# Performance work log

Hardware: AMD Instinct MI355X
Metric: run time of the kernel (lower is better)

## Reference

```python
import jax, jax.numpy as jnp
import numpy as np

B, L, HEADS, D_HEAD = 2, 2048, 16, 64
D_MODEL = HEADS * D_HEAD            # 1024
D_BI = D_MODEL * 4 // 2             # 2048 (bilinear GLU width)
D_PROJ = D_MODEL * 3 + 2 * D_BI
DEPTH = 0                           # block depth < 2 -> token shift active
NEG_INF = -1e10


def _ln(x, g, b, eps=1e-5):
    m = jnp.mean(x, axis=-1, keepdims=True)
    v = jnp.var(x, axis=-1, keepdims=True)
    return (x - m) * jax.lax.rsqrt(v + eps) * g + b


def _shift(x, n):
    # F.pad(x, (0,0,n,-n)): shift along seq dim by n, zero-fill at front
    return jnp.pad(x, ((0, 0), (n, 0), (0, 0)))[:, : x.shape[1], :]


def setup_inputs() -> dict:
    key = jax.random.key(0)
    ks = jax.random.split(key, 3)
    x = jax.random.normal(ks[0], (B, L, D_MODEL), jnp.float32)
    w_in = jax.random.normal(ks[1], (D_MODEL, D_PROJ), jnp.float32) * (D_MODEL ** -0.5)
    # note: torch init zeros out_proj; we use small random weights so backward is non-trivial
    w_out = jax.random.normal(ks[2], (D_MODEL + D_BI, D_MODEL), jnp.float32) * 0.02
    slopes = jnp.concatenate([2.0 ** jnp.linspace(0.0, -6.0, HEADS // 2),
                              jnp.zeros(HEADS - HEADS // 2)]).astype(jnp.float32)
    return {
        "x": x,
        "in_ln_g": jnp.ones(D_MODEL, jnp.float32), "in_ln_b": jnp.zeros(D_MODEL, jnp.float32),
        "mid_ln_g": jnp.ones(D_PROJ, jnp.float32), "mid_ln_b": jnp.zeros(D_PROJ, jnp.float32),
        "out_ln_g": jnp.ones(D_MODEL, jnp.float32), "out_ln_b": jnp.zeros(D_MODEL, jnp.float32),
        "w_in": w_in, "w_out": w_out, "slopes": slopes,
    }


def reference(x, in_ln_g, in_ln_b, mid_ln_g, mid_ln_b, out_ln_g, out_ln_b, w_in, w_out, slopes):
    b, l, d = x.shape
    x = _ln(x, in_ln_g, in_ln_b)
    if DEPTH < 2:
        x = jnp.concatenate([
            _shift(x[..., : d // 4], 1),
            x[..., d // 4: d - d // 8],
            _shift(x[..., d - d // 8:], 2),
        ], axis=-1)
    h = _ln(x @ w_in, mid_ln_g, mid_ln_b)
    q, k, v, p1, p2 = jnp.split(h, [D_MODEL, 2 * D_MODEL, 3 * D_MODEL, 3 * D_MODEL + D_BI], axis=-1)
    to_heads = lambda t: t.reshape(b, l, HEADS, D_HEAD).transpose(0, 2, 1, 3)  # b h l d
    q, k, v = to_heads(q), to_heads(k), to_heads(v)
    logits = jnp.einsum('bhid,bhjd->bhij', q, k) * (D_HEAD ** -0.5)
    pos = jnp.arange(l)
    alibi = pos[None, None, None, :].astype(logits.dtype) * slopes[None, :, None, None]
    causal = jnp.where(pos[:, None] >= pos[None, :], 0.0, NEG_INF).astype(logits.dtype)
    a = jax.nn.softmax(logits + alibi + causal, axis=-1)
    o = jnp.einsum('bhij,bhjd->bhid', a, v).transpose(0, 2, 1, 3).reshape(b, l, d)
    return _ln(jnp.concatenate([o, p1 * p2], axis=-1) @ w_out, out_ln_g, out_ln_b)
```

## Files before the change

### kernel.cpp

```cpp
#include <hip/hip_runtime.h>

#define B_ 2
#define L_ 2048
#define HEADS_ 16
#define DH_ 64
#define DM_ 1024
#define DBI_ 2048
#define DPROJ_ 7168
#define NTOK (B_*L_)
#define DCAT (DM_ + DBI_)

typedef __bf16 bf16;
typedef __attribute__((ext_vector_type(8))) __bf16 bf16x8;
typedef __attribute__((ext_vector_type(4))) float floatx4;

typedef __attribute__((address_space(1))) const void gptr_t;
typedef __attribute__((address_space(3))) void lptr_t;

__device__ __forceinline__ void g2l16(const void* g, void* l) {
    __builtin_amdgcn_global_load_lds((gptr_t*)g, (lptr_t*)l, 16, 0, 0);
}

__global__ __launch_bounds__(256) void transpose_both(const float* __restrict__ w_in,
                                                      const float* __restrict__ w_out,
                                                      bf16* __restrict__ w_inT,
                                                      bf16* __restrict__ w_outT) {
    __shared__ float tile[32][33];
    int l = blockIdx.x;
    const float* in; bf16* outp; int R, C, bx, by;
    if (l < 7168) { in = w_in;  outp = w_inT;  R = DM_;  C = DPROJ_; bx = l % 224; by = l / 224; }
    else { l -= 7168; in = w_out; outp = w_outT; R = DCAT; C = DM_;   bx = l % 32;  by = l / 32; }
    int c0 = bx * 32, r0 = by * 32;
    int x = threadIdx.x & 31, y = threadIdx.x >> 5;
    for (int i = 0; i < 32; i += 8)
        tile[y + i][x] = in[(size_t)(r0 + y + i) * C + (c0 + x)];
    __syncthreads();
    for (int i = 0; i < 32; i += 8)
        outp[(size_t)(c0 + y + i) * R + (r0 + x)] = (bf16)tile[x][y + i];
}

__global__ __launch_bounds__(256) void ln_shift(const float* __restrict__ x,
                                                const float* __restrict__ g,
                                                const float* __restrict__ bb,
                                                bf16* __restrict__ xs) {
    int tok = blockIdx.x;
    int b = tok / L_, l = tok % L_;
    const float* row = x + (size_t)tok * DM_;
    float vals[4];
    float s = 0.f, s2 = 0.f;
    for (int i = 0; i < 4; i++) {
        float v = row[threadIdx.x + i * 256];
        vals[i] = v; s += v; s2 += v * v;
    }
    __shared__ float red[2][4];
    for (int o = 32; o; o >>= 1) { s += __shfl_xor(s, o); s2 += __shfl_xor(s2, o); }
    int w = threadIdx.x >> 6;
    if ((threadIdx.x & 63) == 0) { red[0][w] = s; red[1][w] = s2; }
    __syncthreads();
    s  = red[0][0] + red[0][1] + red[0][2] + red[0][3];
    s2 = red[1][0] + red[1][1] + red[1][2] + red[1][3];
    float mean = s * (1.f / DM_);
    float var  = s2 * (1.f / DM_) - mean * mean;
    float rstd = rsqrtf(var + 1e-5f);
    for (int i = 0; i < 4; i++) {
        int c = threadIdx.x + i * 256;
        float y = (vals[i] - mean) * rstd * g[c] + bb[c];
        int shift = (c < 256) ? 1 : ((c >= 896) ? 2 : 0);
        int dl = l + shift;
        if (dl < L_) xs[((size_t)b * L_ + dl) * DM_ + c] = (bf16)y;
        if (l == 0 && shift) {
            xs[((size_t)b * L_ + 0) * DM_ + c] = (bf16)0.f;
            if (shift == 2) xs[((size_t)b * L_ + 1) * DM_ + c] = (bf16)0.f;
        }
    }
}

__global__ __launch_bounds__(512, 2) void gemm1_fr(const bf16* __restrict__ A,
                                                   const bf16* __restrict__ Bt,
                                                   bf16* __restrict__ C) {
    const int K = DM_, N = DPROJ_;
    int lin = blockIdx.x;
    int xcd = lin & 7, idx = lin >> 3;
    int mt = (xcd >> 2) * 8 + idx / 7;
    int nt = (xcd & 3) * 7 + idx % 7;
    int m0 = mt * 256, n0 = nt * 256;

    __shared__ bf16 As[2][256 * 64];
    __shared__ bf16 Bs[2][256 * 64];

    int t = threadIdx.x;
    int lane = t & 63;
    int c = lane & 15, quad = lane >> 4;
    int wave = t >> 6;
    int wm = (wave >> 2) * 128;
    int wn = (wave & 3) * 64;

    auto stageA = [&](int k0, int bsel, int h) {
        #pragma unroll
        for (int s = 0; s < 2; s++) {
            int g = h * 1024 + s * 512 + t;
            int row = g >> 3;
            int kc = (g & 7) ^ (row & 7);
            g2l16(A + (size_t)(m0 + row) * K + (k0 + kc * 8), &As[bsel][g * 8]);
        }
    };
    auto stageB = [&](int k0, int bsel, int h) {
        #pragma unroll
        for (int s = 0; s < 2; s++) {
            int g = h * 1024 + s * 512 + t;
            int row = g >> 3;
            int kc = (g & 7) ^ (row & 7);
            g2l16(Bt + (size_t)(n0 + row) * K + (k0 + kc * 8), &Bs[bsel][g * 8]);
        }
    };

    floatx4 acc[8][4] = {};

    stageA(0, 0, 0); stageA(0, 0, 1);
    stageB(0, 0, 0); stageB(0, 0, 1);
    stageB(64, 1, 0); stageB(64, 1, 1);
    asm volatile("s_waitcnt vmcnt(4)" ::: "memory");
    __builtin_amdgcn_s_barrier();
    __builtin_amdgcn_sched_barrier(0);

    const int nT = K / 64;
    for (int tt = 0; tt < nT; ++tt) {
        int cur = tt & 1, nxt = cur ^ 1;
        int k1 = (tt + 1) << 6, k2 = (tt + 2) << 6;
        bool dA = (tt + 1 < nT), dB = (tt + 2 < nT);
        bf16x8 bfr[4][2];
        #pragma unroll
        for (int p = 0; p < 4; p++) {
            if      (p == 0) { if (dA) stageA(k1, nxt, 0); }
            else if (p == 1) { if (dA) stageA(k1, nxt, 1); }
            else if (p == 2) { if (dB) stageB(k2, cur, 0); }
            else             { if (dB) stageB(k2, cur, 1); }
            if (p == 0) {
                #pragma unroll
                for (int j = 0; j < 4; j++)
                    #pragma unroll
                    for (int s = 0; s < 2; s++)
                        bfr[j][s] = *(const bf16x8*)&Bs[cur][(wn + j * 16 + c) * 64
                                                            + (((s * 4 + quad) ^ (c & 7)) * 8)];
            }
            bf16x8 af[2][2];
            #pragma unroll
            for (int ii = 0; ii < 2; ii++)
                #pragma unroll
                for (int s = 0; s < 2; s++)
                    af[ii][s] = *(const bf16x8*)&As[cur][(wm + (p * 2 + ii) * 16 + c) * 64
                                                         + (((s * 4 + quad) ^ (c & 7)) * 8)];
            __builtin_amdgcn_s_setprio(1);
            #pragma unroll
            for (int ii = 0; ii < 2; ii++)
                #pragma unroll
                for (int j = 0; j < 4; j++)
                    #pragma unroll
                    for (int s = 0; s < 2; s++)
                        acc[p * 2 + ii][j] = __builtin_amdgcn_mfma_f32_16x16x32_bf16(
                            af[ii][s], bfr[j][s], acc[p * 2 + ii][j], 0, 0, 0);
            __builtin_amdgcn_s_setprio(0);
        }
        asm volatile("s_waitcnt lgkmcnt(0)" ::: "memory");
        if (dB)      { asm volatile("s_waitcnt vmcnt(4)" ::: "memory"); }
        else if (dA) { asm volatile("s_waitcnt vmcnt(0)" ::: "memory"); }
        if (tt + 1 < nT) __builtin_amdgcn_s_barrier();
        __builtin_amdgcn_sched_barrier(0);
    }

    #pragma unroll
    for (int i = 0; i < 8; i++)
        #pragma unroll
        for (int j = 0; j < 4; j++)
            #pragma unroll
            for (int r = 0; r < 4; r++) {
                int row = m0 + wm + i * 16 + quad * 4 + r;
                int col = n0 + wn + j * 16 + c;
                C[(size_t)row * N + col] = (bf16)acc[i][j][r];
            }
}

__global__ __launch_bounds__(256) void gemm2_sk(const bf16* __restrict__ A,
                                                const bf16* __restrict__ Bt,
                                                float* __restrict__ P) {
    const int ldA = DCAT, N = DM_;
    int m0 = blockIdx.x * 128, n0 = blockIdx.y * 128, kz = blockIdx.z;
    const bf16* Ak = A + kz * 1024;
    const bf16* Btk = Bt + kz * 1024;
    float* C = P + (size_t)kz * NTOK * DM_;
    __shared__ bf16 As[2][128 * 32];
    __shared__ bf16 Bs[2][128 * 32];
    int t = threadIdx.x, lane = t & 63, wave = t >> 6;
    int c = lane & 15, quad = lane >> 4;
    int wm = (wave >> 1) * 64, wn = (wave & 1) * 64;
    auto stage = [&](int k0, int bsel) {
        #pragma unroll
        for (int s = 0; s < 2; s++) {
            int f = s * 256 + t;
            int row = f >> 2, kp = (f & 3) * 8;
            g2l16(Ak + (size_t)(m0 + row) * ldA + k0 + kp, &As[bsel][f * 8]);
            g2l16(Btk + (size_t)(n0 + row) * ldA + k0 + kp, &Bs[bsel][f * 8]);
        }
    };
    floatx4 acc[4][4] = {};
    stage(0, 0);
    int buf = 0;
    for (int k0 = 0; k0 < 1024; k0 += 32) {
        __syncthreads();
        if (k0 + 32 < 1024) stage(k0 + 32, buf ^ 1);
        bf16x8 af[4], bfr[4];
        #pragma unroll
        for (int i = 0; i < 4; i++)
            af[i] = *(const bf16x8*)&As[buf][(wm + i * 16 + c) * 32 + quad * 8];
        #pragma unroll
        for (int j = 0; j < 4; j++)
            bfr[j] = *(const bf16x8*)&Bs[buf][(wn + j * 16 + c) * 32 + quad * 8];
        #pragma unroll
        for (int i = 0; i < 4; i++)
            #pragma unroll
            for (int j = 0; j < 4; j++)
                acc[i][j] = __builtin_amdgcn_mfma_f32_16x16x32_bf16(af[i], bfr[j], acc[i][j], 0, 0, 0);
        buf ^= 1;
    }
    #pragma unroll
    for (int i = 0; i < 4; i++)
        #pragma unroll
        for (int j = 0; j < 4; j++)
            #pragma unroll
            for (int r = 0; r < 4; r++) {
                int row = m0 + wm + i * 16 + quad * 4 + r;
                int col = n0 + wn + j * 16 + c;
                C[(size_t)row * N + col] = acc[i][j][r];
            }
}

__global__ __launch_bounds__(256) void mid_ln_fused(const bf16* __restrict__ h,
                                                    const float* __restrict__ g,
                                                    const float* __restrict__ bb,
                                                    bf16* __restrict__ Qp,
                                                    bf16* __restrict__ Kp,
                                                    bf16* __restrict__ Vn,
                                                    bf16* __restrict__ A2) {
    int tok = blockIdx.x;
    int b = tok >> 11, l = tok & 2047;
    size_t base = (size_t)tok * DPROJ_;
    int t = threadIdx.x;
    float v[28];
    float s = 0.f, s2 = 0.f;
    for (int i = 0; i < 28; i++) {
        v[i] = (float)h[base + t + i * 256];
        s += v[i]; s2 += v[i] * v[i];
    }
    __shared__ float red[2][4];
    for (int o = 32; o; o >>= 1) { s += __shfl_xor(s, o); s2 += __shfl_xor(s2, o); }
    int w = t >> 6;
    if ((t & 63) == 0) { red[0][w] = s; red[1][w] = s2; }
    __syncthreads();
    s  = red[0][0] + red[0][1] + red[0][2] + red[0][3];
    s2 = red[1][0] + red[1][1] + red[1][2] + red[1][3];
    float mean = s * (1.f / DPROJ_);
    float var  = s2 * (1.f / DPROJ_) - mean * mean;
    float rstd = rsqrtf(var + 1e-5f);
    #pragma unroll
    for (int i = 0; i < 28; i++) {
        int c = t + i * 256;
        v[i] = (v[i] - mean) * rstd * g[c] + bb[c];
    }
    #pragma unroll
    for (int i = 0; i < 12; i++) {
        int c = t + i * 256;
        int sec = c >> 10;
        int cc = c & 1023;
        int hh = cc >> 6, d = cc & 63;
        size_t idx = (((size_t)b * HEADS_ + hh) * L_ + l) * DH_ + d;
        bf16* dst = (sec == 0) ? Qp : (sec == 1) ? Kp : Vn;
        dst[idx] = (bf16)v[i];
    }
    #pragma unroll
    for (int i = 12; i < 20; i++) {
        int c = t + i * 256;
        A2[(size_t)tok * DCAT + DM_ + (c - 3 * DM_)] = (bf16)(v[i] * v[i + 8]);
    }
}

__global__ __launch_bounds__(256) void vt_pack(const bf16* __restrict__ Vn,
                                               bf16* __restrict__ Vt) {
    __shared__ bf16 tile[32][33];
    int bh = blockIdx.z;
    const bf16* in = Vn + (size_t)bh * L_ * DH_;
    bf16* out = Vt + (size_t)bh * DH_ * L_;
    int l0 = blockIdx.x * 32, d0 = blockIdx.y * 32;
    int x = threadIdx.x & 31, y = threadIdx.x >> 5;
    for (int i = 0; i < 32; i += 8)
        tile[y + i][x] = in[(size_t)(l0 + y + i) * DH_ + d0 + x];
    __syncthreads();
    for (int i = 0; i < 32; i += 8)
        out[(size_t)(d0 + y + i) * L_ + l0 + x] = tile[x][y + i];
}

__global__ __launch_bounds__(256, 4) void attn4(const bf16* __restrict__ Qp,
                                                const bf16* __restrict__ Kp,
                                                const bf16* __restrict__ Vt,
                                                const float* __restrict__ slopes,
                                                bf16* __restrict__ A2) {
    int hd = blockIdx.y, b = blockIdx.z;
    int lin = blockIdx.x + 32 * blockIdx.y + 512 * blockIdx.z;
    int xr = blockIdx.x;
    int qt = ((lin >> 8) & 1) ? (31 - xr) : xr;
    int q0 = qt * 64;
    int t = threadIdx.x, lane = t & 63, wave = t >> 6;
    int quad = lane >> 4, c = lane & 15;
    __shared__ bf16 Ks[2 * 64 * 32];
    __shared__ bf16 Vs[2 * 64 * 32];
    __shared__ bf16 Ps[4][16 * 72];
    int bh = b * HEADS_ + hd;
    const bf16* Qb = Qp + (size_t)bh * L_ * DH_;
    const bf16* Kb = Kp + (size_t)bh * L_ * DH_;
    const bf16* Vb = Vt + (size_t)bh * DH_ * L_;
    const float LOG2E = 1.44269504f;
    float slopeL2 = slopes[hd] * LOG2E;
    const float qscale = 0.125f * LOG2E;

    bf16x8 qf[2];
    int qrow = q0 + wave * 16 + c;
    qf[0] = *(const bf16x8*)(Qb + (size_t)qrow * DH_ + quad * 8);
    qf[1] = *(const bf16x8*)(Qb + (size_t)qrow * DH_ + 32 + quad * 8);
    floatx4 accO[4] = {};
    float lsum[4];
    float mrow[4];
    int i_row0 = q0 + wave * 16 + quad * 4;
    #pragma unroll
    for (int r = 0; r < 4; r++) {
        lsum[r] = 0.f;
        mrow[r] = slopeL2 * (float)(i_row0 + r) + 20.0f;
    }

    int row = t >> 2, kp = (t & 3) * 8;
    bf16* pw = &Ps[wave][0];
    bf16* pwr = pw + (quad * 4) * 72 + c;
    for (int j0 = 0; j0 <= q0; j0 += 64) {
        #pragma unroll
        for (int s = 0; s < 2; s++) {
            g2l16(Kb + (size_t)(j0 + row) * DH_ + s * 32 + kp, &Ks[(s * 256 + t) * 8]);
            g2l16(Vb + (size_t)row * L_ + j0 + s * 32 + kp, &Vs[(s * 256 + t) * 8]);
        }
        __syncthreads();

        bool diag = (j0 == q0);
        #pragma unroll
        for (int nt = 0; nt < 4; nt++) {
            floatx4 sacc = {};
            bf16x8 kf0 = *(const bf16x8*)&Ks[(nt * 16 + c) * 32 + quad * 8];
            bf16x8 kf1 = *(const bf16x8*)&Ks[2048 + (nt * 16 + c) * 32 + quad * 8];
            sacc = __builtin_amdgcn_mfma_f32_16x16x32_bf16(qf[0], kf0, sacc, 0, 0, 0);
            sacc = __builtin_amdgcn_mfma_f32_16x16x32_bf16(qf[1], kf1, sacc, 0, 0, 0);
            int j = j0 + nt * 16 + c;
            float aj = slopeL2 * (float)j;
            #pragma unroll
            for (int r = 0; r < 4; r++) {
                float p = exp2f(fmaf(sacc[r], qscale, aj) - mrow[r]);
                if (diag) p = (j <= i_row0 + r) ? p : 0.f;
                lsum[r] += p;
                pwr[r * 72 + nt * 16] = (bf16)p;
            }
        }
        bf16x8 pf0 = *(const bf16x8*)&pw[c * 72 + quad * 8];
        bf16x8 pf1 = *(const bf16x8*)&pw[c * 72 + 32 + quad * 8];
        #pragma unroll
        for (int nt = 0; nt < 4; nt++) {
            bf16x8 vf0 = *(const bf16x8*)&Vs[(nt * 16 + c) * 32 + quad * 8];
            bf16x8 vf1 = *(const bf16x8*)&Vs[2048 + (nt * 16 + c) * 32 + quad * 8];
            accO[nt] = __builtin_amdgcn_mfma_f32_16x16x32_bf16(pf0, vf0, accO[nt], 0, 0, 0);
            accO[nt] = __builtin_amdgcn_mfma_f32_16x16x32_bf16(pf1, vf1, accO[nt], 0, 0, 0);
        }
        __syncthreads();
    }
    #pragma unroll
    for (int r = 0; r < 4; r++) {
        float l = lsum[r];
        l += __shfl_xor(l, 1);
        l += __shfl_xor(l, 2);
        l += __shfl_xor(l, 4);
        l += __shfl_xor(l, 8);
        lsum[r] = 1.f / l;
    }
    #pragma unroll
    for (int r = 0; r < 4; r++) {
        size_t orow = (size_t)b * L_ + q0 + wave * 16 + quad * 4 + r;
        #pragma unroll
        for (int nt = 0; nt < 4; nt++)
            A2[orow * DCAT + hd * DH_ + nt * 16 + c] = (bf16)(accO[nt][r] * lsum[r]);
    }
}

__global__ __launch_bounds__(256) void out_ln3(const float* __restrict__ P,
                                               const float* __restrict__ g,
                                               const float* __restrict__ bb,
                                               float* __restrict__ out) {
    size_t base = (size_t)blockIdx.x * DM_;
    const size_t stride = (size_t)NTOK * DM_;
    float v[4];
    float s = 0.f, s2 = 0.f;
    for (int i = 0; i < 4; i++) {
        size_t idx = base + threadIdx.x + i * 256;
        v[i] = P[idx] + P[idx + stride] + P[idx + 2 * stride];
        s += v[i]; s2 += v[i] * v[i];
    }
    __shared__ float red[2][4];
    for (int o = 32; o; o >>= 1) { s += __shfl_xor(s, o); s2 += __shfl_xor(s2, o); }
    int w = threadIdx.x >> 6;
    if ((threadIdx.x & 63) == 0) { red[0][w] = s; red[1][w] = s2; }
    __syncthreads();
    s  = red[0][0] + red[0][1] + red[0][2] + red[0][3];
    s2 = red[1][0] + red[1][1] + red[1][2] + red[1][3];
    float mean = s * (1.f / DM_);
    float var  = s2 * (1.f / DM_) - mean * mean;
    float rstd = rsqrtf(var + 1e-5f);
    for (int i = 0; i < 4; i++) {
        int c = threadIdx.x + i * 256;
        out[base + c] = (v[i] - mean) * rstd * g[c] + bb[c];
    }
}

extern "C" void kernel_launch(void* const* d_in, const int* in_sizes, int n_in,
                              void* d_out, int out_size, void* d_ws, size_t ws_size,
                              hipStream_t stream) {
    const float* x     = (const float*)d_in[0];
    const float* in_g  = (const float*)d_in[1];
    const float* in_b  = (const float*)d_in[2];
    const float* mid_g = (const float*)d_in[3];
    const float* mid_b = (const float*)d_in[4];
    const float* out_g = (const float*)d_in[5];
    const float* out_b = (const float*)d_in[6];
    const float* w_in  = (const float*)d_in[7];
    const float* w_out = (const float*)d_in[8];
    const float* slopes = (const float*)d_in[9];
    float* out = (float*)d_out;

    char* ws = (char*)d_ws;
    size_t off = 0;
    auto alloc = [&](size_t n) { char* p = ws + off; off += (n + 255) & ~(size_t)255; return p; };
    bf16* w_inT  = (bf16*)alloc((size_t)DPROJ_ * DM_ * 2);
    bf16* w_outT = (bf16*)alloc((size_t)DM_ * DCAT * 2);
    bf16* xs     = (bf16*)alloc((size_t)NTOK * DM_ * 2);
    bf16* h      = (bf16*)alloc((size_t)NTOK * DPROJ_ * 2);
    bf16* A2     = (bf16*)alloc((size_t)NTOK * DCAT * 2);
    bf16* Qp     = (bf16*)alloc((size_t)NTOK * DM_ * 2);
    bf16* Kp     = (bf16*)alloc((size_t)NTOK * DM_ * 2);
    bf16* Vn     = (bf16*)alloc((size_t)NTOK * DM_ * 2);
    bf16* Vt = xs;
    float* P = (float*)h;

    hipLaunchKernelGGL(transpose_both, dim3(7168 + 3072), dim3(256), 0, stream,
                       w_in, w_out, w_inT, w_outT);
    hipLaunchKernelGGL(ln_shift, dim3(NTOK), dim3(256), 0, stream, x, in_g, in_b, xs);
    hipLaunchKernelGGL(gemm1_fr, dim3(448), dim3(512), 0, stream, xs, w_inT, h);
    hipLaunchKernelGGL(mid_ln_fused, dim3(NTOK), dim3(256), 0, stream, h, mid_g, mid_b,
                       Qp, Kp, Vn, A2);
    hipLaunchKernelGGL(vt_pack, dim3(L_ / 32, DH_ / 32, B_ * HEADS_), dim3(256), 0, stream, Vn, Vt);
    hipLaunchKernelGGL(attn4, dim3(32, HEADS_, B_), dim3(256), 0, stream, Qp, Kp, Vt, slopes, A2);
    hipLaunchKernelGGL(gemm2_sk, dim3(NTOK / 128, DM_ / 128, 3), dim3(256), 0, stream,
                       A2, w_outT, P);
    hipLaunchKernelGGL(out_ln3, dim3(NTOK), dim3(256), 0, stream, P, out_g, out_b, out);
}
```

Before: 309.1 us.

## Restructure gemm1 into a four-slot K=32 ring-buffer pipeline

Replaces the double-buffered K=64 tile pipeline of the first projection GEMM with a four-slot ring of K=32 tiles. Three tiles are prefetched ahead, with a simpler swizzle and one batch of fragment loads per step. The aim is deeper prefetch and fewer stalls waiting on global-to-LDS loads, at the same LDS footprint. In exchange it needs twice as many barriers per K, and each step issues fewer MFMAs between syncs, which could reduce overlap.

```diff
diff --git a/kernel.cpp b/kernel.cpp
--- a/kernel.cpp
+++ b/kernel.cpp
@@ -75,7 +75,7 @@
     }
 }
 
-__global__ __launch_bounds__(512, 2) void gemm1_fr(const bf16* __restrict__ A,
+__global__ __launch_bounds__(512, 2) void gemm1_rg(const bf16* __restrict__ A,
                                                    const bf16* __restrict__ Bt,
                                                    bf16* __restrict__ C) {
     const int K = DM_, N = DPROJ_;
@@ -85,8 +85,8 @@
     int nt = (xcd & 3) * 7 + idx % 7;
     int m0 = mt * 256, n0 = nt * 256;
 
-    __shared__ bf16 As[2][256 * 64];
-    __shared__ bf16 Bs[2][256 * 64];
+    __shared__ bf16 As[4][256 * 32];
+    __shared__ bf16 Bs[4][256 * 32];
 
     int t = threadIdx.x;
     int lane = t & 63;
@@ -95,75 +95,57 @@
     int wm = (wave >> 2) * 128;
     int wn = (wave & 3) * 64;
 
-    auto stageA = [&](int k0, int bsel, int h) {
+    auto stage = [&](int tt) {
+        int k0 = tt << 5, slot = tt & 3;
         #pragma unroll
         for (int s = 0; s < 2; s++) {
-            int g = h * 1024 + s * 512 + t;
-            int row = g >> 3;
-            int kc = (g & 7) ^ (row & 7);
-            g2l16(A + (size_t)(m0 + row) * K + (k0 + kc * 8), &As[bsel][g * 8]);
+            int g = s * 512 + t;
+            int row = g >> 2;
+            int kc = (g & 3) ^ ((g >> 4) & 3);
+            g2l16(A + (size_t)(m0 + row) * K + (k0 + kc * 8), &As[slot][g * 8]);
+        }
+        #pragma unroll
+        for (int s = 0; s < 2; s++) {
+            int g = s * 512 + t;
+            int row = g >> 2;
+            int kc = (g & 3) ^ ((g >> 4) & 3);
+            g2l16(Bt + (size_t)(n0 + row) * K + (k0 + kc * 8), &Bs[slot][g * 8]);
         }
     };
-    auto stageB = [&](int k0, int bsel, int h) {
-        #pragma unroll
-        for (int s = 0; s < 2; s++) {
-            int g = h * 1024 + s * 512 + t;
-            int row = g >> 3;
-            int kc = (g & 7) ^ (row & 7);
-            g2l16(Bt + (size_t)(n0 + row) * K + (k0 + kc * 8), &Bs[bsel][g * 8]);
-        }
-    };
 
     floatx4 acc[8][4] = {};
 
-    stageA(0, 0, 0); stageA(0, 0, 1);
-    stageB(0, 0, 0); stageB(0, 0, 1);
-    stageB(64, 1, 0); stageB(64, 1, 1);
-    asm volatile("s_waitcnt vmcnt(4)" ::: "memory");
+    stage(0); stage(1); stage(2);
+    asm volatile("s_waitcnt vmcnt(8)" ::: "memory");
     __builtin_amdgcn_s_barrier();
     __builtin_amdgcn_sched_barrier(0);
 
-    const int nT = K / 64;
+    const int nT = K / 32;
     for (int tt = 0; tt < nT; ++tt) {
-        int cur = tt & 1, nxt = cur ^ 1;
-        int k1 = (tt + 1) << 6, k2 = (tt + 2) << 6;
-        bool dA = (tt + 1 < nT), dB = (tt + 2 < nT);
-        bf16x8 bfr[4][2];
-        #pragma unroll
-        for (int p = 0; p < 4; p++) {
-            if      (p == 0) { if (dA) stageA(k1, nxt, 0); }
-            else if (p == 1) { if (dA) stageA(k1, nxt, 1); }
-            else if (p == 2) { if (dB) stageB(k2, cur, 0); }
-            else             { if (dB) stageB(k2, cur, 1); }
-            if (p == 0) {
-                #pragma unroll
-                for (int j = 0; j < 4; j++)
-                    #pragma unroll
-                    for (int s = 0; s < 2; s++)
-                        bfr[j][s] = *(const bf16x8*)&Bs[cur][(wn + j * 16 + c) * 64
-                                                            + (((s * 4 + quad) ^ (c & 7)) * 8)];
-            }
-            bf16x8 af[2][2];
+        int slot = tt & 3;
+        if (tt + 3 < nT) stage(tt + 3);
+        bf16x8 af[8], bfr[4];
+        #pragma unroll
+        for (int i = 0; i < 8; i++) {
+            int row = wm + i * 16 + c;
+            af[i] = *(const bf16x8*)&As[slot][row * 32 + ((quad ^ ((row >> 2) & 3)) * 8)];
+        }
+        #pragma unroll
+        for (int j = 0; j < 4; j++) {
+            int row = wn + j * 16 + c;
+            bfr[j] = *(const bf16x8*)&Bs[slot][row * 32 + ((quad ^ ((row >> 2) & 3)) * 8)];
+        }
+        __builtin_amdgcn_s_setprio(1);
+        #pragma unroll
+        for (int i = 0; i < 8; i++)
             #pragma unroll
-            for (int ii = 0; ii < 2; ii++)
-                #pragma unroll
-                for (int s = 0; s < 2; s++)
-                    af[ii][s] = *(const bf16x8*)&As[cur][(wm + (p * 2 + ii) * 16 + c) * 64
-                                                         + (((s * 4 + quad) ^ (c & 7)) * 8)];
-            __builtin_amdgcn_s_setprio(1);
-            #pragma unroll
-            for (int ii = 0; ii < 2; ii++)
-                #pragma unroll
-                for (int j = 0; j < 4; j++)
-                    #pragma unroll
-                    for (int s = 0; s < 2; s++)
-                        acc[p * 2 + ii][j] = __builtin_amdgcn_mfma_f32_16x16x32_bf16(
-                            af[ii][s], bfr[j][s], acc[p * 2 + ii][j], 0, 0, 0);
-            __builtin_amdgcn_s_setprio(0);
-        }
+            for (int j = 0; j < 4; j++)
+                acc[i][j] = __builtin_amdgcn_mfma_f32_16x16x32_bf16(af[i], bfr[j], acc[i][j], 0, 0, 0);
+        __builtin_amdgcn_s_setprio(0);
         asm volatile("s_waitcnt lgkmcnt(0)" ::: "memory");
-        if (dB)      { asm volatile("s_waitcnt vmcnt(4)" ::: "memory"); }
-        else if (dA) { asm volatile("s_waitcnt vmcnt(0)" ::: "memory"); }
+        if (tt + 3 < nT)      { asm volatile("s_waitcnt vmcnt(8)" ::: "memory"); }
+        else if (tt + 2 < nT) { asm volatile("s_waitcnt vmcnt(4)" ::: "memory"); }
+        else if (tt + 1 < nT) { asm volatile("s_waitcnt vmcnt(0)" ::: "memory"); }
         if (tt + 1 < nT) __builtin_amdgcn_s_barrier();
         __builtin_amdgcn_sched_barrier(0);
     }
@@ -454,7 +436,7 @@
     hipLaunchKernelGGL(transpose_both, dim3(7168 + 3072), dim3(256), 0, stream,
                        w_in, w_out, w_inT, w_outT);
     hipLaunchKernelGGL(ln_shift, dim3(NTOK), dim3(256), 0, stream, x, in_g, in_b, xs);
-    hipLaunchKernelGGL(gemm1_fr, dim3(448), dim3(512), 0, stream, xs, w_inT, h);
+    hipLaunchKernelGGL(gemm1_rg, dim3(448), dim3(512), 0, stream, xs, w_inT, h);
     hipLaunchKernelGGL(mid_ln_fused, dim3(NTOK), dim3(256), 0, stream, h, mid_g, mid_b,
                        Qp, Kp, Vn, A2);
     hipLaunchKernelGGL(vt_pack, dim3(L_ / 32, DH_ / 32, B_ * HEADS_), dim3(256), 0, stream, Vn, Vt);
```

New measurement: 330.3 us. +6.9%, slower.

## Load attention K/V fragments directly from global memory and remap block-to-XCD order

Applied to the files above, without the earlier changes.

The attention kernel stops staging K and V tiles in shared memory with block-wide barriers. Each wave now reads its MFMA K and V fragments straight from global memory and relies on the cache for reuse across the four waves. Block IDs are also remapped so that consecutive IDs land on the same (fid&7) group, which presumably keeps work for a given head on one XCD's L2. This removes the LDS round-trip and both __syncthreads per iteration. In exchange, each wave issues redundant global loads, and the loads are exposed with no prefetch, so they could stall the wave.

```diff
diff --git a/kernel.cpp b/kernel.cpp
--- a/kernel.cpp
+++ b/kernel.cpp
@@ -298,20 +298,17 @@
         out[(size_t)(d0 + y + i) * L_ + l0 + x] = tile[x][y + i];
 }
 
-__global__ __launch_bounds__(256, 4) void attn4(const bf16* __restrict__ Qp,
+__global__ __launch_bounds__(256, 4) void attn5(const bf16* __restrict__ Qp,
                                                 const bf16* __restrict__ Kp,
                                                 const bf16* __restrict__ Vt,
                                                 const float* __restrict__ slopes,
                                                 bf16* __restrict__ A2) {
-    int hd = blockIdx.y, b = blockIdx.z;
-    int lin = blockIdx.x + 32 * blockIdx.y + 512 * blockIdx.z;
-    int xr = blockIdx.x;
-    int qt = ((lin >> 8) & 1) ? (31 - xr) : xr;
+    int fid = blockIdx.x + 32 * blockIdx.y + 512 * blockIdx.z;
+    int wl = (fid & 7) * 128 + (fid >> 3);
+    int qt = wl & 31, hd = (wl >> 5) & 15, b = wl >> 9;
     int q0 = qt * 64;
     int t = threadIdx.x, lane = t & 63, wave = t >> 6;
     int quad = lane >> 4, c = lane & 15;
-    __shared__ bf16 Ks[2 * 64 * 32];
-    __shared__ bf16 Vs[2 * 64 * 32];
     __shared__ bf16 Ps[4][16 * 72];
     int bh = b * HEADS_ + hd;
     const bf16* Qb = Qp + (size_t)bh * L_ * DH_;
@@ -335,23 +332,16 @@
         mrow[r] = slopeL2 * (float)(i_row0 + r) + 20.0f;
     }
 
-    int row = t >> 2, kp = (t & 3) * 8;
     bf16* pw = &Ps[wave][0];
     bf16* pwr = pw + (quad * 4) * 72 + c;
     for (int j0 = 0; j0 <= q0; j0 += 64) {
-        #pragma unroll
-        for (int s = 0; s < 2; s++) {
-            g2l16(Kb + (size_t)(j0 + row) * DH_ + s * 32 + kp, &Ks[(s * 256 + t) * 8]);
-            g2l16(Vb + (size_t)row * L_ + j0 + s * 32 + kp, &Vs[(s * 256 + t) * 8]);
-        }
-        __syncthreads();
-
         bool diag = (j0 == q0);
         #pragma unroll
         for (int nt = 0; nt < 4; nt++) {
+            const bf16* kb = Kb + (size_t)(j0 + nt * 16 + c) * DH_ + quad * 8;
+            bf16x8 kf0 = *(const bf16x8*)(kb);
+            bf16x8 kf1 = *(const bf16x8*)(kb + 32);
             floatx4 sacc = {};
-            bf16x8 kf0 = *(const bf16x8*)&Ks[(nt * 16 + c) * 32 + quad * 8];
-            bf16x8 kf1 = *(const bf16x8*)&Ks[2048 + (nt * 16 + c) * 32 + quad * 8];
             sacc = __builtin_amdgcn_mfma_f32_16x16x32_bf16(qf[0], kf0, sacc, 0, 0, 0);
             sacc = __builtin_amdgcn_mfma_f32_16x16x32_bf16(qf[1], kf1, sacc, 0, 0, 0);
             int j = j0 + nt * 16 + c;
@@ -368,12 +358,12 @@
         bf16x8 pf1 = *(const bf16x8*)&pw[c * 72 + 32 + quad * 8];
         #pragma unroll
         for (int nt = 0; nt < 4; nt++) {
-            bf16x8 vf0 = *(const bf16x8*)&Vs[(nt * 16 + c) * 32 + quad * 8];
-            bf16x8 vf1 = *(const bf16x8*)&Vs[2048 + (nt * 16 + c) * 32 + quad * 8];
+            const bf16* vb = Vb + (size_t)(nt * 16 + c) * L_ + j0 + quad * 8;
+            bf16x8 vf0 = *(const bf16x8*)(vb);
+            bf16x8 vf1 = *(const bf16x8*)(vb + 32);
             accO[nt] = __builtin_amdgcn_mfma_f32_16x16x32_bf16(pf0, vf0, accO[nt], 0, 0, 0);
             accO[nt] = __builtin_amdgcn_mfma_f32_16x16x32_bf16(pf1, vf1, accO[nt], 0, 0, 0);
         }
-        __syncthreads();
     }
     #pragma unroll
     for (int r = 0; r < 4; r++) {
@@ -458,7 +448,7 @@
     hipLaunchKernelGGL(mid_ln_fused, dim3(NTOK), dim3(256), 0, stream, h, mid_g, mid_b,
                        Qp, Kp, Vn, A2);
     hipLaunchKernelGGL(vt_pack, dim3(L_ / 32, DH_ / 32, B_ * HEADS_), dim3(256), 0, stream, Vn, Vt);
-    hipLaunchKernelGGL(attn4, dim3(32, HEADS_, B_), dim3(256), 0, stream, Qp, Kp, Vt, slopes, A2);
+    hipLaunchKernelGGL(attn5, dim3(32, HEADS_, B_), dim3(256), 0, stream, Qp, Kp, Vt, slopes, A2);
     hipLaunchKernelGGL(gemm2_sk, dim3(NTOK / 128, DM_ / 128, 3), dim3(256), 0, stream,
                        A2, w_outT, P);
     hipLaunchKernelGGL(out_ln3, dim3(NTOK), dim3(256), 0, stream, P, out_g, out_b, out);
```

Result: slower. 484.0 us (+56.6%).

## Double-buffer K tiles and overlap V loads with QK^T in attention

Applied to the files above, without the earlier changes.

The attention kernel now prefetches the next K tile into a second LDS buffer while computing the current scores. The V tile load is issued at the start of each iteration and only waited on before the PV MFMAs, with explicit vmcnt waits and raw barriers in place of __syncthreads. The goal is to hide global-to-LDS latency behind the softmax and MFMA work. In exchange the kernel uses more LDS (an extra 8KB K buffer) and depends on hand-written waitcnt accounting for correctness.

```diff
diff --git a/kernel.cpp b/kernel.cpp
--- a/kernel.cpp
+++ b/kernel.cpp
@@ -298,7 +298,7 @@
         out[(size_t)(d0 + y + i) * L_ + l0 + x] = tile[x][y + i];
 }
 
-__global__ __launch_bounds__(256, 4) void attn4(const bf16* __restrict__ Qp,
+__global__ __launch_bounds__(256, 4) void attn6(const bf16* __restrict__ Qp,
                                                 const bf16* __restrict__ Kp,
                                                 const bf16* __restrict__ Vt,
                                                 const float* __restrict__ slopes,
@@ -310,8 +310,8 @@
     int q0 = qt * 64;
     int t = threadIdx.x, lane = t & 63, wave = t >> 6;
     int quad = lane >> 4, c = lane & 15;
-    __shared__ bf16 Ks[2 * 64 * 32];
-    __shared__ bf16 Vs[2 * 64 * 32];
+    __shared__ bf16 Ks[2][64 * 64];
+    __shared__ bf16 Vs[64 * 64];
     __shared__ bf16 Ps[4][16 * 72];
     int bh = b * HEADS_ + hd;
     const bf16* Qb = Qp + (size_t)bh * L_ * DH_;
@@ -336,22 +336,37 @@
     }
 
     int row = t >> 2, kp = (t & 3) * 8;
+    auto stageK = [&](int j0, int kb) {
+        #pragma unroll
+        for (int s = 0; s < 2; s++)
+            g2l16(Kb + (size_t)(j0 + row) * DH_ + s * 32 + kp, &Ks[kb][(s * 256 + t) * 8]);
+    };
+    auto stageV = [&](int j0) {
+        #pragma unroll
+        for (int s = 0; s < 2; s++)
+            g2l16(Vb + (size_t)row * L_ + j0 + s * 32 + kp, &Vs[(s * 256 + t) * 8]);
+    };
+
     bf16* pw = &Ps[wave][0];
     bf16* pwr = pw + (quad * 4) * 72 + c;
+
+    stageK(0, 0);
+    asm volatile("s_waitcnt vmcnt(0)" ::: "memory");
+    __builtin_amdgcn_s_barrier();
+    __builtin_amdgcn_sched_barrier(0);
+
+    int kb = 0;
     for (int j0 = 0; j0 <= q0; j0 += 64) {
-        #pragma unroll
-        for (int s = 0; s < 2; s++) {
-            g2l16(Kb + (size_t)(j0 + row) * DH_ + s * 32 + kp, &Ks[(s * 256 + t) * 8]);
-            g2l16(Vb + (size_t)row * L_ + j0 + s * 32 + kp, &Vs[(s * 256 + t) * 8]);
-        }
-        __syncthreads();
+        bool dK = (j0 + 64 <= q0);
+        stageV(j0);
+        if (dK) stageK(j0 + 64, kb ^ 1);
 
         bool diag = (j0 == q0);
         #pragma unroll
         for (int nt = 0; nt < 4; nt++) {
             floatx4 sacc = {};
-            bf16x8 kf0 = *(const bf16x8*)&Ks[(nt * 16 + c) * 32 + quad * 8];
-            bf16x8 kf1 = *(const bf16x8*)&Ks[2048 + (nt * 16 + c) * 32 + quad * 8];
+            bf16x8 kf0 = *(const bf16x8*)&Ks[kb][(nt * 16 + c) * 32 + quad * 8];
+            bf16x8 kf1 = *(const bf16x8*)&Ks[kb][2048 + (nt * 16 + c) * 32 + quad * 8];
             sacc = __builtin_amdgcn_mfma_f32_16x16x32_bf16(qf[0], kf0, sacc, 0, 0, 0);
             sacc = __builtin_amdgcn_mfma_f32_16x16x32_bf16(qf[1], kf1, sacc, 0, 0, 0);
             int j = j0 + nt * 16 + c;
@@ -366,6 +381,12 @@
         }
         bf16x8 pf0 = *(const bf16x8*)&pw[c * 72 + quad * 8];
         bf16x8 pf1 = *(const bf16x8*)&pw[c * 72 + 32 + quad * 8];
+
+        if (dK) { asm volatile("s_waitcnt vmcnt(2)" ::: "memory"); }
+        else    { asm volatile("s_waitcnt vmcnt(0)" ::: "memory"); }
+        __builtin_amdgcn_s_barrier();
+        __builtin_amdgcn_sched_barrier(0);
+
         #pragma unroll
         for (int nt = 0; nt < 4; nt++) {
             bf16x8 vf0 = *(const bf16x8*)&Vs[(nt * 16 + c) * 32 + quad * 8];
@@ -373,7 +394,10 @@
             accO[nt] = __builtin_amdgcn_mfma_f32_16x16x32_bf16(pf0, vf0, accO[nt], 0, 0, 0);
             accO[nt] = __builtin_amdgcn_mfma_f32_16x16x32_bf16(pf1, vf1, accO[nt], 0, 0, 0);
         }
-        __syncthreads();
+        asm volatile("s_waitcnt lgkmcnt(0)" ::: "memory");
+        __builtin_amdgcn_s_barrier();
+        __builtin_amdgcn_sched_barrier(0);
+        kb ^= 1;
     }
     #pragma unroll
     for (int r = 0; r < 4; r++) {
@@ -458,7 +482,7 @@
     hipLaunchKernelGGL(mid_ln_fused, dim3(NTOK), dim3(256), 0, stream, h, mid_g, mid_b,
                        Qp, Kp, Vn, A2);
     hipLaunchKernelGGL(vt_pack, dim3(L_ / 32, DH_ / 32, B_ * HEADS_), dim3(256), 0, stream, Vn, Vt);
-    hipLaunchKernelGGL(attn4, dim3(32, HEADS_, B_), dim3(256), 0, stream, Qp, Kp, Vt, slopes, A2);
+    hipLaunchKernelGGL(attn6, dim3(32, HEADS_, B_), dim3(256), 0, stream, Qp, Kp, Vt, slopes, A2);
     hipLaunchKernelGGL(gemm2_sk, dim3(NTOK / 128, DM_ / 128, 3), dim3(256), 0, stream,
                        A2, w_outT, P);
     hipLaunchKernelGGL(out_ln3, dim3(NTOK), dim3(256), 0, stream, P, out_g, out_b, out);
```

After: 307.1 us. About the same (-0.6%).
